# Kernel optimization log

Hardware: AMD Instinct MI355X
Metric: run time of the kernel (lower is better)

Reference implementation:

```python
import jax, jax.numpy as jnp
import numpy as np

N = 100000
E = 1600000
D_IN = 128
D_OUT = 128
EPS = 1e-5


def setup_inputs() -> dict:
    key = jax.random.key(0)
    ks = jax.random.split(key, 8)
    x = jax.random.normal(ks[0], (N, D_IN), dtype=jnp.float32)
    edge_index = jax.random.randint(ks[1], (2, E), 0, N, dtype=jnp.int64)
    s1 = 1.0 / np.sqrt(D_IN)
    s2 = 1.0 / np.sqrt(D_OUT)
    W1 = jax.random.uniform(ks[2], (D_IN, D_OUT), jnp.float32, -s1, s1)
    b1 = jax.random.uniform(ks[3], (D_OUT,), jnp.float32, -s1, s1)
    W2 = jax.random.uniform(ks[4], (D_OUT, D_OUT), jnp.float32, -s2, s2)
    b2 = jax.random.uniform(ks[5], (D_OUT,), jnp.float32, -s2, s2)
    gamma = jnp.ones((D_OUT,), jnp.float32)
    beta = jnp.zeros((D_OUT,), jnp.float32)
    return {"x": x, "edge_index": edge_index, "W1": W1, "b1": b1,
            "W2": W2, "b2": b2, "gamma": gamma, "beta": beta}


def reference(x, edge_index, W1, b1, W2, b2, gamma, beta):
    row, col = edge_index[0], edge_index[1]
    # scatter-add neighbor aggregation: agg[row] += x[col]
    agg = jax.ops.segment_sum(x[col], row, num_segments=N)
    h = x + agg  # residual (self) + aggregated neighbors
    # MLP: Linear -> ReLU -> Linear -> BatchNorm1d (training-mode batch stats)
    h = jax.nn.relu(h @ W1 + b1)
    h = h @ W2 + b2
    mean = jnp.mean(h, axis=0)
    var = jnp.mean(jnp.square(h - mean), axis=0)  # biased var, as torch BN uses
    out = gamma * (h - mean) * jax.lax.rsqrt(var + EPS) + beta
    return out
```

## Files before the change

### kernel.cpp

```cpp
#include <hip/hip_runtime.h>

#define N_NODES 100000
#define N_EDGES 1600000
#define DIM     128
#define EPS_BN  1e-5f
#define NB      512
#define NPB     196
#define NBLK    256
#define EPB     6250
#define CAP     4096
#define M_TILE  64
#define M_PAD   100032
#define GBLK    1563
#define LPITCH  136

typedef __attribute__((ext_vector_type(8))) short short8;
typedef __attribute__((ext_vector_type(4))) float floatx4;

__device__ __forceinline__ unsigned short f2bf(float f) {
    unsigned u = __float_as_uint(f);
    return (unsigned short)((u + 0x7FFF + ((u >> 16) & 1)) >> 16);
}
__device__ __forceinline__ float bf2f(unsigned short b) {
    return __uint_as_float((unsigned)b << 16);
}

__device__ __forceinline__ int detect64(const void* eidx) {
    int v = ((const int*)eidx)[2 * (threadIdx.x & 63) + 1];
    unsigned long long b = __ballot(v != 0);
    return (b == 0ULL) ? 1 : 0;
}
__device__ __forceinline__ int load_row(const void* eidx, int is64, int e) {
    if (is64) return (int)((const long long*)eidx)[e];
    return ((const int*)eidx)[e];
}
__device__ __forceinline__ int load_col(const void* eidx, int is64, int e) {
    if (is64) return (int)((const long long*)eidx)[N_EDGES + e];
    return ((const int*)eidx)[N_EDGES + e];
}

__global__ void convert_w(const float* __restrict__ W1,
                          const float* __restrict__ W2,
                          unsigned short* __restrict__ W1t,
                          unsigned short* __restrict__ W2t,
                          int* __restrict__ bcur, float* __restrict__ gstats) {
    if (blockIdx.x == 2) {
        int t = threadIdx.x;
        if (t < NB) bcur[t] = 0;
        if (t < 256) { if (t < NB - 256) bcur[256 + t] = 0; }
        bcur[256 + threadIdx.x] = 0;
        if (t < 2 * DIM) gstats[t] = 0.f;
        return;
    }
    const float* W = blockIdx.x ? W2 : W1;
    unsigned short* Wt = blockIdx.x ? W2t : W1t;
    for (int i = threadIdx.x; i < DIM * DIM; i += 256) {
        int k = i >> 7, n = i & 127;
        Wt[n * DIM + k] = f2bf(W[i]);
    }
}

__global__ __launch_bounds__(256) void bin_scatter(const void* eidx, int* bcur,
                                                   unsigned* __restrict__ slots) {
    __shared__ int lh[NB];
    __shared__ int lbase[NB];
    __shared__ int loff[NB];
    __shared__ unsigned stage[EPB];
    __shared__ int gaddr[EPB];
    int t = threadIdx.x;
    int is64 = detect64(eidx);
    lh[t] = 0; lh[t + 256] = 0;
    __syncthreads();
    int base = blockIdx.x * EPB;
    for (int i = t; i < EPB; i += 256) {
        int r = load_row(eidx, is64, base + i);
        atomicAdd(&lh[r / NPB], 1);
    }
    __syncthreads();
    loff[t] = lh[t]; loff[t + 256] = lh[t + 256];
    __syncthreads();
    for (int off = 1; off < NB; off <<= 1) {
        int a0 = (t >= off) ? loff[t - off] : 0;
        int a1 = (t + 256 >= off) ? loff[t + 256 - off] : 0;
        __syncthreads();
        loff[t] += a0; loff[t + 256] += a1;
        __syncthreads();
    }
#pragma unroll
    for (int q = 0; q < 2; ++q) {
        int i = t + 256 * q;
        int c = lh[i];
        lbase[i] = c ? atomicAdd(&bcur[i], c) : 0;
        loff[i] -= c;
        lh[i] = 0;
    }
    __syncthreads();
    for (int i = t; i < EPB; i += 256) {
        int r = load_row(eidx, is64, base + i);
        int c = load_col(eidx, is64, base + i);
        int b = r / NPB;
        int pos = atomicAdd(&lh[b], 1);
        int idx = loff[b] + pos;
        stage[idx] = ((unsigned)(r - b * NPB) << 24) | (unsigned)c;
        gaddr[idx] = b * CAP + lbase[b] + pos;
    }
    __syncthreads();
    for (int i = t; i < EPB; i += 256)
        slots[gaddr[i]] = stage[i];
}

__global__ __launch_bounds__(256) void build_csr(const unsigned* __restrict__ slots,
                                                 const int* __restrict__ bcnt,
                                                 int* __restrict__ rowst,
                                                 int* __restrict__ cols) {
    __shared__ int tmp[NB];
    __shared__ int hist[256];
    __shared__ int excl[256];
    __shared__ int cur[256];
    __shared__ int colbuf[CAP];
    int t = threadIdx.x;
    int b = blockIdx.x;
    tmp[t] = bcnt[t]; tmp[t + 256] = bcnt[t + 256];
    __syncthreads();
    for (int off = 1; off < NB; off <<= 1) {
        int a0 = (t >= off) ? tmp[t - off] : 0;
        int a1 = (t + 256 >= off) ? tmp[t + 256 - off] : 0;
        __syncthreads();
        tmp[t] += a0; tmp[t + 256] += a1;
        __syncthreads();
    }
    int cnt = bcnt[b];
    int s = tmp[b] - cnt;
    int node0 = b * NPB;
    int nn = N_NODES - node0;
    if (nn > NPB) nn = NPB;
    const unsigned* pairs = slots + (size_t)b * CAP;
    hist[t] = 0;
    if (b == NB - 1 && t == 0) rowst[N_NODES] = N_EDGES;
    __syncthreads();
    for (int i = t; i < cnt; i += 256)
        atomicAdd(&hist[(int)(pairs[i] >> 24)], 1);
    __syncthreads();
    int v = hist[t];
    excl[t] = v;
    __syncthreads();
    for (int off = 1; off < 256; off <<= 1) {
        int a = (t >= off) ? excl[t - off] : 0;
        __syncthreads();
        excl[t] += a;
        __syncthreads();
    }
    int ex = excl[t] - v;
    if (t < nn) rowst[node0 + t] = s + ex;
    cur[t] = ex;
    __syncthreads();
    for (int i = t; i < cnt; i += 256) {
        unsigned pr = pairs[i];
        int pos = atomicAdd(&cur[pr >> 24], 1);
        colbuf[pos] = (int)(pr & 0xFFFFFFu);
    }
    __syncthreads();
    for (int i = t; i < cnt; i += 256) cols[s + i] = colbuf[i];
}

__global__ void xconv(const float* __restrict__ x,
                      unsigned short* __restrict__ xb) {
    int i = blockIdx.x * 256 + threadIdx.x;
    float4 v = ((const float4*)x)[i];
    ushort4 o;
    o.x = f2bf(v.x); o.y = f2bf(v.y); o.z = f2bf(v.z); o.w = f2bf(v.w);
    ((ushort4*)xb)[i] = o;
}

__global__ __launch_bounds__(256) void agg_kernel(
    const unsigned short* __restrict__ xb,
    const int* __restrict__ row_start, const int* __restrict__ cols,
    unsigned short* __restrict__ Hbf) {
    int wave = threadIdx.x >> 6;
    int lane = threadIdx.x & 63;
    int node = blockIdx.x * 4 + wave;
    const unsigned* xbw = (const unsigned*)xb;
    unsigned selfw = xbw[(size_t)node * 64 + lane];
    float2 acc;
    acc.x = __uint_as_float(selfw << 16);
    acc.y = __uint_as_float(selfw & 0xffff0000u);
    int s = row_start[node], e = row_start[node + 1];
    s = __builtin_amdgcn_readfirstlane(s);
    e = __builtin_amdgcn_readfirstlane(e);
    int d = e - s;
    if (d <= 16) {
        unsigned pw[16];
#pragma unroll
        for (int u = 0; u < 16; ++u) {
            int idx = s + u;
            int ci = (idx < e) ? idx : s;
            pw[u] = xbw[(size_t)cols[ci] * 64 + lane];
        }
#pragma unroll
        for (int u = 0; u < 16; ++u) {
            unsigned w = (u < d) ? pw[u] : 0u;
            acc.x += __uint_as_float(w << 16);
            acc.y += __uint_as_float(w & 0xffff0000u);
        }
    } else if (d <= 32) {
        unsigned pw[32];
#pragma unroll
        for (int u = 0; u < 32; ++u) {
            int idx = s + u;
            int ci = (idx < e) ? idx : s;
            pw[u] = xbw[(size_t)cols[ci] * 64 + lane];
        }
#pragma unroll
        for (int u = 0; u < 32; ++u) {
            unsigned w = (u < d) ? pw[u] : 0u;
            acc.x += __uint_as_float(w << 16);
            acc.y += __uint_as_float(w & 0xffff0000u);
        }
    } else {
        int j = s;
        for (; j + 16 <= e; j += 16) {
            unsigned pw[16];
#pragma unroll
            for (int u = 0; u < 16; ++u)
                pw[u] = xbw[(size_t)cols[j + u] * 64 + lane];
#pragma unroll
            for (int u = 0; u < 16; ++u) {
                acc.x += __uint_as_float(pw[u] << 16);
                acc.y += __uint_as_float(pw[u] & 0xffff0000u);
            }
        }
        for (; j < e; ++j) {
            unsigned pv = xbw[(size_t)cols[j] * 64 + lane];
            acc.x += __uint_as_float(pv << 16);
            acc.y += __uint_as_float(pv & 0xffff0000u);
        }
    }
    unsigned pack = (unsigned)f2bf(acc.x) | ((unsigned)f2bf(acc.y) << 16);
    ((unsigned*)Hbf)[(size_t)node * 64 + lane] = pack;
}

__global__ __launch_bounds__(256) void mlp_fused(
    const unsigned short* __restrict__ A,
    const unsigned short* __restrict__ B1t,
    const unsigned short* __restrict__ B2t,
    const float* __restrict__ bias1, const float* __restrict__ bias2,
    unsigned short* __restrict__ outb,
    float* __restrict__ gpart) {
    __shared__ unsigned short As[M_TILE * LPITCH];
    __shared__ unsigned short Bs[DIM * LPITCH];
    int t = threadIdx.x;
    int row0 = blockIdx.x * M_TILE;
    int lane = t & 63, wv = t >> 6;
    int m = lane & 15, g = lane >> 4;

#pragma unroll
    for (int i = 0; i < 4; ++i) {
        int ch = t + 256 * i;
        int r = ch >> 4, cc = ch & 15;
        *(uint4*)(&As[r * LPITCH + cc * 8]) =
            *(const uint4*)(&A[(size_t)(row0 + r) * DIM + cc * 8]);
    }
#pragma unroll
    for (int i = 0; i < 8; ++i) {
        int ch = t + 256 * i;
        int n = ch >> 4, cc = ch & 15;
        *(uint4*)(&Bs[n * LPITCH + cc * 8]) =
            *(const uint4*)(&B1t[n * DIM + cc * 8]);
    }
    __syncthreads();

    floatx4 acc1[8] = {};
#pragma unroll
    for (int kc = 0; kc < 4; ++kc) {
        short8 a = *(const short8*)(&As[(wv * 16 + m) * LPITCH + kc * 32 + g * 8]);
#pragma unroll
        for (int tt = 0; tt < 8; ++tt) {
            short8 b = *(const short8*)(&Bs[(tt * 16 + m) * LPITCH + kc * 32 + g * 8]);
            acc1[tt] = __builtin_amdgcn_mfma_f32_16x16x32_bf16(a, b, acc1[tt], 0, 0, 0);
        }
    }
    __syncthreads();

    uint4 wbuf[8];
#pragma unroll
    for (int i = 0; i < 8; ++i) {
        int ch = t + 256 * i;
        int n = ch >> 4, cc = ch & 15;
        wbuf[i] = *(const uint4*)(&B2t[n * DIM + cc * 8]);
    }
#pragma unroll
    for (int tt = 0; tt < 8; ++tt) {
        int col = tt * 16 + m;
        float bv = bias1[col];
#pragma unroll
        for (int j = 0; j < 4; ++j) {
            int rl = wv * 16 + g * 4 + j;
            As[rl * LPITCH + col] = f2bf(fmaxf(acc1[tt][j] + bv, 0.f));
        }
    }
#pragma unroll
    for (int i = 0; i < 8; ++i) {
        int ch = t + 256 * i;
        int n = ch >> 4, cc = ch & 15;
        *(uint4*)(&Bs[n * LPITCH + cc * 8]) = wbuf[i];
    }
    __syncthreads();

    floatx4 acc2[8] = {};
#pragma unroll
    for (int kc = 0; kc < 4; ++kc) {
        short8 a = *(const short8*)(&As[(wv * 16 + m) * LPITCH + kc * 32 + g * 8]);
#pragma unroll
        for (int tt = 0; tt < 8; ++tt) {
            short8 b = *(const short8*)(&Bs[(tt * 16 + m) * LPITCH + kc * 32 + g * 8]);
            acc2[tt] = __builtin_amdgcn_mfma_f32_16x16x32_bf16(a, b, acc2[tt], 0, 0, 0);
        }
    }

    float* csum = (float*)As;
    float* csq = csum + DIM;
    __syncthreads();
    if (t < DIM) { csum[t] = 0.f; csq[t] = 0.f; }
    __syncthreads();
#pragma unroll
    for (int tt = 0; tt < 8; ++tt) {
        int col = tt * 16 + m;
        float bv = bias2[col];
        float s = 0.f, q = 0.f;
#pragma unroll
        for (int j = 0; j < 4; ++j) {
            int row = row0 + wv * 16 + g * 4 + j;
            float v = acc2[tt][j] + bv;
            outb[(size_t)row * DIM + col] = f2bf(v);
            if (row < N_NODES) { s += v; q += v * v; }
        }
        atomicAdd(&csum[col], s);
        atomicAdd(&csq[col], q);
    }
    __syncthreads();
    gpart[(size_t)blockIdx.x * 256 + t] = (t < DIM) ? csum[t] : csq[t - DIM];
}

__global__ __launch_bounds__(256) void reduce_stats(
    const float* __restrict__ gpart, float* __restrict__ gstats) {
    int t = threadIdx.x;
    int chunk = (GBLK + 31) / 32;
    int r0 = blockIdx.x * chunk;
    int r1 = r0 + chunk < GBLK ? r0 + chunk : GBLK;
    float s = 0.f;
    for (int r = r0; r < r1; ++r) s += gpart[(size_t)r * 256 + t];
    atomicAdd(&gstats[t], s);
}

__global__ __launch_bounds__(256) void bn_apply(
    const unsigned short* __restrict__ H2, const float* __restrict__ gstats,
    const float* __restrict__ gamma, const float* __restrict__ beta,
    float* __restrict__ out) {
    __shared__ float sc_s[DIM], sh_s[DIM];
    int t = threadIdx.x;
    if (t < DIM) {
        float mean = gstats[t] * (1.0f / N_NODES);
        float m2 = gstats[DIM + t] * (1.0f / N_NODES);
        float var = m2 - mean * mean;
        float inv = rsqrtf(var + EPS_BN);
        float sc = gamma[t] * inv;
        sc_s[t] = sc;
        sh_s[t] = beta[t] - mean * sc;
    }
    __syncthreads();
    int i = blockIdx.x * 256 + t;
    int j4 = (i & 31) * 4;
    ushort4 hv = ((const ushort4*)H2)[i];
    float4 o;
    o.x = bf2f(hv.x) * sc_s[j4 + 0] + sh_s[j4 + 0];
    o.y = bf2f(hv.y) * sc_s[j4 + 1] + sh_s[j4 + 1];
    o.z = bf2f(hv.z) * sc_s[j4 + 2] + sh_s[j4 + 2];
    o.w = bf2f(hv.w) * sc_s[j4 + 3] + sh_s[j4 + 3];
    ((float4*)out)[i] = o;
}

extern "C" void kernel_launch(void* const* d_in, const int* in_sizes, int n_in,
                              void* d_out, int out_size, void* d_ws,
                              size_t ws_size, hipStream_t stream) {
    (void)in_sizes; (void)n_in; (void)out_size; (void)ws_size;
    const float* x     = (const float*)d_in[0];
    const void*  eidx  = d_in[1];
    const float* W1    = (const float*)d_in[2];
    const float* b1    = (const float*)d_in[3];
    const float* W2    = (const float*)d_in[4];
    const float* b2    = (const float*)d_in[5];
    const float* gamma = (const float*)d_in[6];
    const float* beta  = (const float*)d_in[7];
    float* out = (float*)d_out;

    char* p = (char*)d_ws;
    auto alloc = [&](size_t bytes) {
        char* r = p;
        p += (bytes + 255) & ~(size_t)255;
        return r;
    };
    unsigned short* Hbf  = (unsigned short*)alloc((size_t)M_PAD * DIM * 2);
    unsigned short* h2bf = (unsigned short*)alloc((size_t)M_PAD * DIM * 2);
    unsigned* slots = (unsigned*)h2bf;
    unsigned short* xb = (unsigned short*)alloc((size_t)N_NODES * DIM * 2);
    int*   cols   = (int*)alloc((size_t)(N_EDGES + 64) * 4);
    float* gpart  = (float*)alloc((size_t)GBLK * 256 * 4);
    int*   rowst  = (int*)alloc((size_t)(N_NODES + 1) * 4);
    int*   bcur   = (int*)alloc(NB * 4);
    unsigned short* W1t = (unsigned short*)alloc(DIM * DIM * 2);
    unsigned short* W2t = (unsigned short*)alloc(DIM * DIM * 2);
    float* gstats = (float*)alloc(2 * DIM * 4);

    convert_w<<<3, 256, 0, stream>>>(W1, W2, W1t, W2t, bcur, gstats);
    bin_scatter<<<NBLK, 256, 0, stream>>>(eidx, bcur, slots);
    build_csr<<<NB, 256, 0, stream>>>(slots, bcur, rowst, cols);

    xconv<<<N_NODES * DIM / 4 / 256, 256, 0, stream>>>(x, xb);
    agg_kernel<<<N_NODES / 4, 256, 0, stream>>>(xb, rowst, cols, Hbf);

    mlp_fused<<<GBLK, 256, 0, stream>>>(Hbf, W1t, W2t, b1, b2, h2bf, gpart);
    reduce_stats<<<32, 256, 0, stream>>>(gpart, gstats);
    bn_apply<<<(N_NODES * DIM / 4) / 256, 256, 0, stream>>>(h2bf, gstats,
                                                            gamma, beta, out);
}
```

Baseline: 312.0 us.

## Fuse neighbor aggregation into MLP kernel and merge x and weight conversion

The CSR gather-aggregation now runs inside the MLP kernel: each wave aggregates 16 nodes one after another and writes the bf16 result straight into the LDS A-tile. This removes the intermediate Hbf buffer and its global write and read-back, plus one kernel launch. The x-to-bf16 conversion is also merged with the weight transpose and counter zeroing into one launch. In exchange, far fewer waves are in flight for the latency-bound gather (1563 blocks with a large LDS footprint instead of 25000 small blocks), and each wave's node loop is serial, which can hide memory latency less well.

```diff
diff --git a/kernel.cpp b/kernel.cpp
--- a/kernel.cpp
+++ b/kernel.cpp
@@ -39,24 +39,30 @@
     return ((const int*)eidx)[N_EDGES + e];
 }
 
-__global__ void convert_w(const float* __restrict__ W1,
-                          const float* __restrict__ W2,
-                          unsigned short* __restrict__ W1t,
-                          unsigned short* __restrict__ W2t,
-                          int* __restrict__ bcur, float* __restrict__ gstats) {
-    if (blockIdx.x == 2) {
+__global__ void xconv_w(const float* __restrict__ x,
+                        unsigned short* __restrict__ xb,
+                        const float* __restrict__ W1,
+                        const float* __restrict__ W2,
+                        unsigned short* __restrict__ W1t,
+                        unsigned short* __restrict__ W2t,
+                        int* __restrict__ bcur, float* __restrict__ gstats) {
+    int i = blockIdx.x * 256 + threadIdx.x;
+    float4 v = ((const float4*)x)[i];
+    ushort4 o;
+    o.x = f2bf(v.x); o.y = f2bf(v.y); o.z = f2bf(v.z); o.w = f2bf(v.w);
+    ((ushort4*)xb)[i] = o;
+    if (blockIdx.x < 2) {
+        const float* W = blockIdx.x ? W2 : W1;
+        unsigned short* Wt = blockIdx.x ? W2t : W1t;
+        for (int j = threadIdx.x; j < DIM * DIM; j += 256) {
+            int k = j >> 7, n = j & 127;
+            Wt[n * DIM + k] = f2bf(W[j]);
+        }
+    } else if (blockIdx.x == 2) {
         int t = threadIdx.x;
-        if (t < NB) bcur[t] = 0;
-        if (t < 256) { if (t < NB - 256) bcur[256 + t] = 0; }
-        bcur[256 + threadIdx.x] = 0;
+        bcur[t] = 0;
+        bcur[256 + t] = 0;
         if (t < 2 * DIM) gstats[t] = 0.f;
-        return;
-    }
-    const float* W = blockIdx.x ? W2 : W1;
-    unsigned short* Wt = blockIdx.x ? W2t : W1t;
-    for (int i = threadIdx.x; i < DIM * DIM; i += 256) {
-        int k = i >> 7, n = i & 127;
-        Wt[n * DIM + k] = f2bf(W[i]);
     }
 }
 
@@ -163,84 +169,9 @@
     for (int i = t; i < cnt; i += 256) cols[s + i] = colbuf[i];
 }
 
-__global__ void xconv(const float* __restrict__ x,
-                      unsigned short* __restrict__ xb) {
-    int i = blockIdx.x * 256 + threadIdx.x;
-    float4 v = ((const float4*)x)[i];
-    ushort4 o;
-    o.x = f2bf(v.x); o.y = f2bf(v.y); o.z = f2bf(v.z); o.w = f2bf(v.w);
-    ((ushort4*)xb)[i] = o;
-}
-
-__global__ __launch_bounds__(256) void agg_kernel(
+__global__ __launch_bounds__(256) void agg_mlp(
     const unsigned short* __restrict__ xb,
     const int* __restrict__ row_start, const int* __restrict__ cols,
-    unsigned short* __restrict__ Hbf) {
-    int wave = threadIdx.x >> 6;
-    int lane = threadIdx.x & 63;
-    int node = blockIdx.x * 4 + wave;
-    const unsigned* xbw = (const unsigned*)xb;
-    unsigned selfw = xbw[(size_t)node * 64 + lane];
-    float2 acc;
-    acc.x = __uint_as_float(selfw << 16);
-    acc.y = __uint_as_float(selfw & 0xffff0000u);
-    int s = row_start[node], e = row_start[node + 1];
-    s = __builtin_amdgcn_readfirstlane(s);
-    e = __builtin_amdgcn_readfirstlane(e);
-    int d = e - s;
-    if (d <= 16) {
-        unsigned pw[16];
-#pragma unroll
-        for (int u = 0; u < 16; ++u) {
-            int idx = s + u;
-            int ci = (idx < e) ? idx : s;
-            pw[u] = xbw[(size_t)cols[ci] * 64 + lane];
-        }
-#pragma unroll
-        for (int u = 0; u < 16; ++u) {
-            unsigned w = (u < d) ? pw[u] : 0u;
-            acc.x += __uint_as_float(w << 16);
-            acc.y += __uint_as_float(w & 0xffff0000u);
-        }
-    } else if (d <= 32) {
-        unsigned pw[32];
-#pragma unroll
-        for (int u = 0; u < 32; ++u) {
-            int idx = s + u;
-            int ci = (idx < e) ? idx : s;
-            pw[u] = xbw[(size_t)cols[ci] * 64 + lane];
-        }
-#pragma unroll
-        for (int u = 0; u < 32; ++u) {
-            unsigned w = (u < d) ? pw[u] : 0u;
-            acc.x += __uint_as_float(w << 16);
-            acc.y += __uint_as_float(w & 0xffff0000u);
-        }
-    } else {
-        int j = s;
-        for (; j + 16 <= e; j += 16) {
-            unsigned pw[16];
-#pragma unroll
-            for (int u = 0; u < 16; ++u)
-                pw[u] = xbw[(size_t)cols[j + u] * 64 + lane];
-#pragma unroll
-            for (int u = 0; u < 16; ++u) {
-                acc.x += __uint_as_float(pw[u] << 16);
-                acc.y += __uint_as_float(pw[u] & 0xffff0000u);
-            }
-        }
-        for (; j < e; ++j) {
-            unsigned pv = xbw[(size_t)cols[j] * 64 + lane];
-            acc.x += __uint_as_float(pv << 16);
-            acc.y += __uint_as_float(pv & 0xffff0000u);
-        }
-    }
-    unsigned pack = (unsigned)f2bf(acc.x) | ((unsigned)f2bf(acc.y) << 16);
-    ((unsigned*)Hbf)[(size_t)node * 64 + lane] = pack;
-}
-
-__global__ __launch_bounds__(256) void mlp_fused(
-    const unsigned short* __restrict__ A,
     const unsigned short* __restrict__ B1t,
     const unsigned short* __restrict__ B2t,
     const float* __restrict__ bias1, const float* __restrict__ bias2,
@@ -254,18 +185,76 @@
     int m = lane & 15, g = lane >> 4;
 
 #pragma unroll
-    for (int i = 0; i < 4; ++i) {
-        int ch = t + 256 * i;
-        int r = ch >> 4, cc = ch & 15;
-        *(uint4*)(&As[r * LPITCH + cc * 8]) =
-            *(const uint4*)(&A[(size_t)(row0 + r) * DIM + cc * 8]);
-    }
-#pragma unroll
     for (int i = 0; i < 8; ++i) {
         int ch = t + 256 * i;
         int n = ch >> 4, cc = ch & 15;
         *(uint4*)(&Bs[n * LPITCH + cc * 8]) =
             *(const uint4*)(&B1t[n * DIM + cc * 8]);
+    }
+
+    const unsigned* xbw = (const unsigned*)xb;
+    for (int r = 0; r < 16; ++r) {
+        int node = row0 + wv * 16 + r;
+        unsigned pack = 0u;
+        if (node < N_NODES) {
+            unsigned selfw = xbw[(size_t)node * 64 + lane];
+            float2 acc;
+            acc.x = __uint_as_float(selfw << 16);
+            acc.y = __uint_as_float(selfw & 0xffff0000u);
+            int s = row_start[node], e = row_start[node + 1];
+            s = __builtin_amdgcn_readfirstlane(s);
+            e = __builtin_amdgcn_readfirstlane(e);
+            int d = e - s;
+            if (d <= 16) {
+                unsigned pw[16];
+#pragma unroll
+                for (int u = 0; u < 16; ++u) {
+                    int idx = s + u;
+                    int ci = (idx < e) ? idx : s;
+                    pw[u] = xbw[(size_t)cols[ci] * 64 + lane];
+                }
+#pragma unroll
+                for (int u = 0; u < 16; ++u) {
+                    unsigned w = (u < d) ? pw[u] : 0u;
+                    acc.x += __uint_as_float(w << 16);
+                    acc.y += __uint_as_float(w & 0xffff0000u);
+                }
+            } else if (d <= 32) {
+                unsigned pw[32];
+#pragma unroll
+                for (int u = 0; u < 32; ++u) {
+                    int idx = s + u;
+                    int ci = (idx < e) ? idx : s;
+                    pw[u] = xbw[(size_t)cols[ci] * 64 + lane];
+                }
+#pragma unroll
+                for (int u = 0; u < 32; ++u) {
+                    unsigned w = (u < d) ? pw[u] : 0u;
+                    acc.x += __uint_as_float(w << 16);
+                    acc.y += __uint_as_float(w & 0xffff0000u);
+                }
+            } else {
+                int j = s;
+                for (; j + 16 <= e; j += 16) {
+                    unsigned pw[16];
+#pragma unroll
+                    for (int u = 0; u < 16; ++u)
+                        pw[u] = xbw[(size_t)cols[j + u] * 64 + lane];
+#pragma unroll
+                    for (int u = 0; u < 16; ++u) {
+                        acc.x += __uint_as_float(pw[u] << 16);
+                        acc.y += __uint_as_float(pw[u] & 0xffff0000u);
+                    }
+                }
+                for (; j < e; ++j) {
+                    unsigned pv = xbw[(size_t)cols[j] * 64 + lane];
+                    acc.x += __uint_as_float(pv << 16);
+                    acc.y += __uint_as_float(pv & 0xffff0000u);
+                }
+            }
+            pack = (unsigned)f2bf(acc.x) | ((unsigned)f2bf(acc.y) << 16);
+        }
+        *(unsigned*)(&As[(wv * 16 + r) * LPITCH + lane * 2]) = pack;
     }
     __syncthreads();
 
@@ -399,7 +388,6 @@
         p += (bytes + 255) & ~(size_t)255;
         return r;
     };
-    unsigned short* Hbf  = (unsigned short*)alloc((size_t)M_PAD * DIM * 2);
     unsigned short* h2bf = (unsigned short*)alloc((size_t)M_PAD * DIM * 2);
     unsigned* slots = (unsigned*)h2bf;
     unsigned short* xb = (unsigned short*)alloc((size_t)N_NODES * DIM * 2);
@@ -411,14 +399,13 @@
     unsigned short* W2t = (unsigned short*)alloc(DIM * DIM * 2);
     float* gstats = (float*)alloc(2 * DIM * 4);
 
-    convert_w<<<3, 256, 0, stream>>>(W1, W2, W1t, W2t, bcur, gstats);
+    xconv_w<<<N_NODES * DIM / 4 / 256, 256, 0, stream>>>(x, xb, W1, W2,
+                                                         W1t, W2t, bcur, gstats);
     bin_scatter<<<NBLK, 256, 0, stream>>>(eidx, bcur, slots);
     build_csr<<<NB, 256, 0, stream>>>(slots, bcur, rowst, cols);
 
-    xconv<<<N_NODES * DIM / 4 / 256, 256, 0, stream>>>(x, xb);
-    agg_kernel<<<N_NODES / 4, 256, 0, stream>>>(xb, rowst, cols, Hbf);
-
-    mlp_fused<<<GBLK, 256, 0, stream>>>(Hbf, W1t, W2t, b1, b2, h2bf, gpart);
+    agg_mlp<<<GBLK, 256, 0, stream>>>(xb, rowst, cols, W1t, W2t, b1, b2,
+                                      h2bf, gpart);
     reduce_stats<<<32, 256, 0, stream>>>(gpart, gstats);
     bn_apply<<<(N_NODES * DIM / 4) / 256, 256, 0, stream>>>(h2bf, gstats,
                                                             gamma, beta, out);
```

Result: slower. 326.4 us (+4.6%).

## Make MLP kernel persistent with prefetched tiles and fuse x conversion into binning

Applied to the files above, without the earlier changes.

The MLP kernel becomes persistent with 256 blocks. Each block loads both weight matrices into LDS once, double-buffers the A tiles with a register prefetch of the next tile, and accumulates BN statistics in registers across its tiles, so the reduce-stats pass has fewer partials. The separate x-to-bf16 conversion kernel is folded into the tail of the bin-scatter kernel to save one launch and overlap with the scatter work. In exchange, LDS use rises to about 104KB per block, which limits occupancy, and only 256 blocks may underfill the GPU's compute units.

```diff
diff --git a/kernel.cpp b/kernel.cpp
--- a/kernel.cpp
+++ b/kernel.cpp
@@ -12,6 +12,7 @@
 #define M_TILE  64
 #define M_PAD   100032
 #define GBLK    1563
+#define PBLK    256
 #define LPITCH  136
 
 typedef __attribute__((ext_vector_type(8))) short short8;
@@ -46,9 +47,8 @@
                           int* __restrict__ bcur, float* __restrict__ gstats) {
     if (blockIdx.x == 2) {
         int t = threadIdx.x;
-        if (t < NB) bcur[t] = 0;
-        if (t < 256) { if (t < NB - 256) bcur[256 + t] = 0; }
-        bcur[256 + threadIdx.x] = 0;
+        bcur[t] = 0;
+        bcur[256 + t] = 0;
         if (t < 2 * DIM) gstats[t] = 0.f;
         return;
     }
@@ -60,8 +60,9 @@
     }
 }
 
-__global__ __launch_bounds__(256) void bin_scatter(const void* eidx, int* bcur,
-                                                   unsigned* __restrict__ slots) {
+__global__ __launch_bounds__(256) void bin_scatter_x(
+    const void* eidx, int* bcur, unsigned* __restrict__ slots,
+    const float* __restrict__ x, unsigned short* __restrict__ xb) {
     __shared__ int lh[NB];
     __shared__ int lbase[NB];
     __shared__ int loff[NB];
@@ -107,6 +108,12 @@
     __syncthreads();
     for (int i = t; i < EPB; i += 256)
         slots[gaddr[i]] = stage[i];
+    for (int i = blockIdx.x * 256 + t; i < N_NODES * DIM / 4; i += NBLK * 256) {
+        float4 v = ((const float4*)x)[i];
+        ushort4 o;
+        o.x = f2bf(v.x); o.y = f2bf(v.y); o.z = f2bf(v.z); o.w = f2bf(v.w);
+        ((ushort4*)xb)[i] = o;
+    }
 }
 
 __global__ __launch_bounds__(256) void build_csr(const unsigned* __restrict__ slots,
@@ -161,15 +168,6 @@
     }
     __syncthreads();
     for (int i = t; i < cnt; i += 256) cols[s + i] = colbuf[i];
-}
-
-__global__ void xconv(const float* __restrict__ x,
-                      unsigned short* __restrict__ xb) {
-    int i = blockIdx.x * 256 + threadIdx.x;
-    float4 v = ((const float4*)x)[i];
-    ushort4 o;
-    o.x = f2bf(v.x); o.y = f2bf(v.y); o.z = f2bf(v.z); o.w = f2bf(v.w);
-    ((ushort4*)xb)[i] = o;
 }
 
 __global__ __launch_bounds__(256) void agg_kernel(
@@ -239,82 +237,105 @@
     ((unsigned*)Hbf)[(size_t)node * 64 + lane] = pack;
 }
 
-__global__ __launch_bounds__(256) void mlp_fused(
+__global__ __launch_bounds__(256) void mlp_persist(
     const unsigned short* __restrict__ A,
     const unsigned short* __restrict__ B1t,
     const unsigned short* __restrict__ B2t,
     const float* __restrict__ bias1, const float* __restrict__ bias2,
     unsigned short* __restrict__ outb,
     float* __restrict__ gpart) {
-    __shared__ unsigned short As[M_TILE * LPITCH];
-    __shared__ unsigned short Bs[DIM * LPITCH];
+    __shared__ unsigned short As[2][M_TILE * LPITCH];
+    __shared__ unsigned short Bs1[DIM * LPITCH];
+    __shared__ unsigned short Bs2[DIM * LPITCH];
     int t = threadIdx.x;
-    int row0 = blockIdx.x * M_TILE;
     int lane = t & 63, wv = t >> 6;
     int m = lane & 15, g = lane >> 4;
-
-#pragma unroll
-    for (int i = 0; i < 4; ++i) {
-        int ch = t + 256 * i;
-        int r = ch >> 4, cc = ch & 15;
-        *(uint4*)(&As[r * LPITCH + cc * 8]) =
-            *(const uint4*)(&A[(size_t)(row0 + r) * DIM + cc * 8]);
-    }
+    int r_ = t >> 4, c_ = t & 15;
+
 #pragma unroll
     for (int i = 0; i < 8; ++i) {
         int ch = t + 256 * i;
         int n = ch >> 4, cc = ch & 15;
-        *(uint4*)(&Bs[n * LPITCH + cc * 8]) =
-            *(const uint4*)(&B1t[n * DIM + cc * 8]);
-    }
-    __syncthreads();
-
-    floatx4 acc1[8] = {};
-#pragma unroll
-    for (int kc = 0; kc < 4; ++kc) {
-        short8 a = *(const short8*)(&As[(wv * 16 + m) * LPITCH + kc * 32 + g * 8]);
+        *(uint4*)(&Bs1[n * LPITCH + cc * 8]) = *(const uint4*)(&B1t[n * DIM + cc * 8]);
+        *(uint4*)(&Bs2[n * LPITCH + cc * 8]) = *(const uint4*)(&B2t[n * DIM + cc * 8]);
+    }
+    int tl = blockIdx.x;
+    {
+        int row0 = tl * M_TILE;
+#pragma unroll
+        for (int i = 0; i < 4; ++i)
+            *(uint4*)(&As[0][(r_ + 16 * i) * LPITCH + c_ * 8]) =
+                *(const uint4*)(&A[(size_t)(row0 + r_ + 16 * i) * DIM + c_ * 8]);
+    }
+    float bv1[8], bv2[8];
+#pragma unroll
+    for (int tt = 0; tt < 8; ++tt) {
+        bv1[tt] = bias1[tt * 16 + m];
+        bv2[tt] = bias2[tt * 16 + m];
+    }
+    float bsum[8] = {}, bsq[8] = {};
+    __syncthreads();
+
+    int cur = 0;
+    while (tl < GBLK) {
+        int nxt = tl + PBLK;
+        bool pf = (nxt < GBLK);
+        uint4 ald[4];
+        if (pf) {
+            int row0n = nxt * M_TILE;
+#pragma unroll
+            for (int i = 0; i < 4; ++i)
+                ald[i] = *(const uint4*)(&A[(size_t)(row0n + r_ + 16 * i) * DIM + c_ * 8]);
+        }
+        floatx4 acc1[8] = {};
+#pragma unroll
+        for (int kc = 0; kc < 4; ++kc) {
+            short8 a = *(const short8*)(&As[cur][(wv * 16 + m) * LPITCH + kc * 32 + g * 8]);
+#pragma unroll
+            for (int tt = 0; tt < 8; ++tt) {
+                short8 b = *(const short8*)(&Bs1[(tt * 16 + m) * LPITCH + kc * 32 + g * 8]);
+                acc1[tt] = __builtin_amdgcn_mfma_f32_16x16x32_bf16(a, b, acc1[tt], 0, 0, 0);
+            }
+        }
+        __syncthreads();
 #pragma unroll
         for (int tt = 0; tt < 8; ++tt) {
-            short8 b = *(const short8*)(&Bs[(tt * 16 + m) * LPITCH + kc * 32 + g * 8]);
-            acc1[tt] = __builtin_amdgcn_mfma_f32_16x16x32_bf16(a, b, acc1[tt], 0, 0, 0);
-        }
-    }
-    __syncthreads();
-
-    uint4 wbuf[8];
-#pragma unroll
-    for (int i = 0; i < 8; ++i) {
-        int ch = t + 256 * i;
-        int n = ch >> 4, cc = ch & 15;
-        wbuf[i] = *(const uint4*)(&B2t[n * DIM + cc * 8]);
-    }
-#pragma unroll
-    for (int tt = 0; tt < 8; ++tt) {
-        int col = tt * 16 + m;
-        float bv = bias1[col];
-#pragma unroll
-        for (int j = 0; j < 4; ++j) {
-            int rl = wv * 16 + g * 4 + j;
-            As[rl * LPITCH + col] = f2bf(fmaxf(acc1[tt][j] + bv, 0.f));
-        }
-    }
-#pragma unroll
-    for (int i = 0; i < 8; ++i) {
-        int ch = t + 256 * i;
-        int n = ch >> 4, cc = ch & 15;
-        *(uint4*)(&Bs[n * LPITCH + cc * 8]) = wbuf[i];
-    }
-    __syncthreads();
-
-    floatx4 acc2[8] = {};
-#pragma unroll
-    for (int kc = 0; kc < 4; ++kc) {
-        short8 a = *(const short8*)(&As[(wv * 16 + m) * LPITCH + kc * 32 + g * 8]);
+            int col = tt * 16 + m;
+#pragma unroll
+            for (int j = 0; j < 4; ++j) {
+                int rl = wv * 16 + g * 4 + j;
+                As[cur][rl * LPITCH + col] = f2bf(fmaxf(acc1[tt][j] + bv1[tt], 0.f));
+            }
+        }
+        if (pf) {
+#pragma unroll
+            for (int i = 0; i < 4; ++i)
+                *(uint4*)(&As[cur ^ 1][(r_ + 16 * i) * LPITCH + c_ * 8]) = ald[i];
+        }
+        __syncthreads();
+        floatx4 acc2[8] = {};
+#pragma unroll
+        for (int kc = 0; kc < 4; ++kc) {
+            short8 a = *(const short8*)(&As[cur][(wv * 16 + m) * LPITCH + kc * 32 + g * 8]);
+#pragma unroll
+            for (int tt = 0; tt < 8; ++tt) {
+                short8 b = *(const short8*)(&Bs2[(tt * 16 + m) * LPITCH + kc * 32 + g * 8]);
+                acc2[tt] = __builtin_amdgcn_mfma_f32_16x16x32_bf16(a, b, acc2[tt], 0, 0, 0);
+            }
+        }
+        int row0 = tl * M_TILE;
 #pragma unroll
         for (int tt = 0; tt < 8; ++tt) {
-            short8 b = *(const short8*)(&Bs[(tt * 16 + m) * LPITCH + kc * 32 + g * 8]);
-            acc2[tt] = __builtin_amdgcn_mfma_f32_16x16x32_bf16(a, b, acc2[tt], 0, 0, 0);
-        }
+            int col = tt * 16 + m;
+#pragma unroll
+            for (int j = 0; j < 4; ++j) {
+                int row = row0 + wv * 16 + g * 4 + j;
+                float v = acc2[tt][j] + bv2[tt];
+                outb[(size_t)row * DIM + col] = f2bf(v);
+                if (row < N_NODES) { bsum[tt] += v; bsq[tt] += v * v; }
+            }
+        }
+        tl = nxt; cur ^= 1;
     }
 
     float* csum = (float*)As;
@@ -324,18 +345,8 @@
     __syncthreads();
 #pragma unroll
     for (int tt = 0; tt < 8; ++tt) {
-        int col = tt * 16 + m;
-        float bv = bias2[col];
-        float s = 0.f, q = 0.f;
-#pragma unroll
-        for (int j = 0; j < 4; ++j) {
-            int row = row0 + wv * 16 + g * 4 + j;
-            float v = acc2[tt][j] + bv;
-            outb[(size_t)row * DIM + col] = f2bf(v);
-            if (row < N_NODES) { s += v; q += v * v; }
-        }
-        atomicAdd(&csum[col], s);
-        atomicAdd(&csq[col], q);
+        atomicAdd(&csum[tt * 16 + m], bsum[tt]);
+        atomicAdd(&csq[tt * 16 + m], bsq[tt]);
     }
     __syncthreads();
     gpart[(size_t)blockIdx.x * 256 + t] = (t < DIM) ? csum[t] : csq[t - DIM];
@@ -344,11 +355,9 @@
 __global__ __launch_bounds__(256) void reduce_stats(
     const float* __restrict__ gpart, float* __restrict__ gstats) {
     int t = threadIdx.x;
-    int chunk = (GBLK + 31) / 32;
-    int r0 = blockIdx.x * chunk;
-    int r1 = r0 + chunk < GBLK ? r0 + chunk : GBLK;
+    int r0 = blockIdx.x * (PBLK / 32);
     float s = 0.f;
-    for (int r = r0; r < r1; ++r) s += gpart[(size_t)r * 256 + t];
+    for (int r = r0; r < r0 + PBLK / 32; ++r) s += gpart[(size_t)r * 256 + t];
     atomicAdd(&gstats[t], s);
 }
 
@@ -404,7 +413,7 @@
     unsigned* slots = (unsigned*)h2bf;
     unsigned short* xb = (unsigned short*)alloc((size_t)N_NODES * DIM * 2);
     int*   cols   = (int*)alloc((size_t)(N_EDGES + 64) * 4);
-    float* gpart  = (float*)alloc((size_t)GBLK * 256 * 4);
+    float* gpart  = (float*)alloc((size_t)PBLK * 256 * 4);
     int*   rowst  = (int*)alloc((size_t)(N_NODES + 1) * 4);
     int*   bcur   = (int*)alloc(NB * 4);
     unsigned short* W1t = (unsigned short*)alloc(DIM * DIM * 2);
@@ -412,13 +421,12 @@
     float* gstats = (float*)alloc(2 * DIM * 4);
 
     convert_w<<<3, 256, 0, stream>>>(W1, W2, W1t, W2t, bcur, gstats);
-    bin_scatter<<<NBLK, 256, 0, stream>>>(eidx, bcur, slots);
+    bin_scatter_x<<<NBLK, 256, 0, stream>>>(eidx, bcur, slots, x, xb);
     build_csr<<<NB, 256, 0, stream>>>(slots, bcur, rowst, cols);
 
-    xconv<<<N_NODES * DIM / 4 / 256, 256, 0, stream>>>(x, xb);
     agg_kernel<<<N_NODES / 4, 256, 0, stream>>>(xb, rowst, cols, Hbf);
 
-    mlp_fused<<<GBLK, 256, 0, stream>>>(Hbf, W1t, W2t, b1, b2, h2bf, gpart);
+    mlp_persist<<<PBLK, 256, 0, stream>>>(Hbf, W1t, W2t, b1, b2, h2bf, gpart);
     reduce_stats<<<32, 256, 0, stream>>>(gpart, gstats);
     bn_apply<<<(N_NODES * DIM / 4) / 256, 256, 0, stream>>>(h2bf, gstats,
                                                             gamma, beta, out);
```

Result: no change. 309.2 us (-0.9%).

## Replace bucketed CSR build with degree histogram, scan, and atomic scatter

Applied to the files above, without the earlier changes.

Replaces the two-pass bucket binning CSR construction (shared-memory staging into fixed-capacity slots, then a per-bucket local sort) with a global per-node degree histogram via atomics, a two-kernel prefix scan, and a direct atomic scatter of column indices. The x-to-bf16 conversion, weight transposition and zeroing are folded into a single init kernel. The aim is to cut the staged buffer traffic and shared-memory-heavy low-occupancy kernels. In exchange it relies on 1.6M global atomics on random addresses, and the order of neighbours within a row becomes nondeterministic.

```diff
diff --git a/kernel.cpp b/kernel.cpp
--- a/kernel.cpp
+++ b/kernel.cpp
@@ -4,15 +4,12 @@
 #define N_EDGES 1600000
 #define DIM     128
 #define EPS_BN  1e-5f
-#define NB      512
-#define NPB     196
-#define NBLK    256
-#define EPB     6250
-#define CAP     4096
 #define M_TILE  64
 #define M_PAD   100032
 #define GBLK    1563
 #define LPITCH  136
+#define EGRID   2048
+#define CHUNK   391
 
 typedef __attribute__((ext_vector_type(8))) short short8;
 typedef __attribute__((ext_vector_type(4))) float floatx4;
@@ -39,137 +36,113 @@
     return ((const int*)eidx)[N_EDGES + e];
 }
 
-__global__ void convert_w(const float* __restrict__ W1,
-                          const float* __restrict__ W2,
-                          unsigned short* __restrict__ W1t,
-                          unsigned short* __restrict__ W2t,
-                          int* __restrict__ bcur, float* __restrict__ gstats) {
-    if (blockIdx.x == 2) {
-        int t = threadIdx.x;
-        if (t < NB) bcur[t] = 0;
-        if (t < 256) { if (t < NB - 256) bcur[256 + t] = 0; }
-        bcur[256 + threadIdx.x] = 0;
+__global__ __launch_bounds__(256) void init_all(
+    const float* __restrict__ x, unsigned short* __restrict__ xb,
+    const float* __restrict__ W1, const float* __restrict__ W2,
+    unsigned short* __restrict__ W1t, unsigned short* __restrict__ W2t,
+    int* __restrict__ deg, float* __restrict__ gstats) {
+    int t = threadIdx.x;
+    for (int i = blockIdx.x * 256 + t; i < N_NODES * DIM / 4; i += EGRID * 256) {
+        float4 v = ((const float4*)x)[i];
+        ushort4 o;
+        o.x = f2bf(v.x); o.y = f2bf(v.y); o.z = f2bf(v.z); o.w = f2bf(v.w);
+        ((ushort4*)xb)[i] = o;
+    }
+    if (blockIdx.x < 2) {
+        const float* W = blockIdx.x ? W2 : W1;
+        unsigned short* Wt = blockIdx.x ? W2t : W1t;
+        for (int j = t; j < DIM * DIM; j += 256) {
+            int k = j >> 7, n = j & 127;
+            Wt[n * DIM + k] = f2bf(W[j]);
+        }
+    } else if (blockIdx.x == 2) {
         if (t < 2 * DIM) gstats[t] = 0.f;
-        return;
-    }
-    const float* W = blockIdx.x ? W2 : W1;
-    unsigned short* Wt = blockIdx.x ? W2t : W1t;
-    for (int i = threadIdx.x; i < DIM * DIM; i += 256) {
-        int k = i >> 7, n = i & 127;
-        Wt[n * DIM + k] = f2bf(W[i]);
-    }
-}
-
-__global__ __launch_bounds__(256) void bin_scatter(const void* eidx, int* bcur,
-                                                   unsigned* __restrict__ slots) {
-    __shared__ int lh[NB];
-    __shared__ int lbase[NB];
-    __shared__ int loff[NB];
-    __shared__ unsigned stage[EPB];
-    __shared__ int gaddr[EPB];
-    int t = threadIdx.x;
+    } else if (blockIdx.x >= 3 && blockIdx.x < 103) {
+        int base = (blockIdx.x - 3) * 1024;
+#pragma unroll
+        for (int k = 0; k < 4; ++k) {
+            int i = base + k * 256 + t;
+            if (i < N_NODES) deg[i] = 0;
+        }
+    }
+}
+
+__global__ __launch_bounds__(256) void edge_hist(const void* eidx,
+                                                 int* __restrict__ deg) {
     int is64 = detect64(eidx);
-    lh[t] = 0; lh[t + 256] = 0;
-    __syncthreads();
-    int base = blockIdx.x * EPB;
-    for (int i = t; i < EPB; i += 256) {
-        int r = load_row(eidx, is64, base + i);
-        atomicAdd(&lh[r / NPB], 1);
-    }
-    __syncthreads();
-    loff[t] = lh[t]; loff[t + 256] = lh[t + 256];
-    __syncthreads();
-    for (int off = 1; off < NB; off <<= 1) {
-        int a0 = (t >= off) ? loff[t - off] : 0;
-        int a1 = (t + 256 >= off) ? loff[t + 256 - off] : 0;
+    for (int e = blockIdx.x * 256 + threadIdx.x; e < N_EDGES; e += EGRID * 256)
+        atomicAdd(&deg[load_row(eidx, is64, e)], 1);
+}
+
+__global__ __launch_bounds__(256) void scan_part(const int* __restrict__ deg,
+                                                 int* __restrict__ bsum) {
+    __shared__ int red[256];
+    int t = threadIdx.x;
+    int n0 = blockIdx.x * CHUNK;
+    int s = 0;
+    int i0 = n0 + t, i1 = n0 + t + 256;
+    if (t < CHUNK && i0 < N_NODES) s += deg[i0];
+    if (t + 256 < CHUNK && i1 < N_NODES) s += deg[i1];
+    red[t] = s;
+    __syncthreads();
+    for (int off = 128; off > 0; off >>= 1) {
+        if (t < off) red[t] += red[t + off];
         __syncthreads();
-        loff[t] += a0; loff[t + 256] += a1;
+    }
+    if (t == 0) bsum[blockIdx.x] = red[0];
+}
+
+__global__ __launch_bounds__(256) void scan_write(const int* __restrict__ deg,
+                                                  const int* __restrict__ bsum,
+                                                  int* __restrict__ rowst,
+                                                  int* __restrict__ cur) {
+    __shared__ int bs[256];
+    __shared__ int ch[512];
+    int t = threadIdx.x;
+    int b = blockIdx.x;
+    bs[t] = bsum[t];
+    __syncthreads();
+    for (int off = 1; off < 256; off <<= 1) {
+        int a = (t >= off) ? bs[t - off] : 0;
         __syncthreads();
-    }
-#pragma unroll
-    for (int q = 0; q < 2; ++q) {
-        int i = t + 256 * q;
-        int c = lh[i];
-        lbase[i] = c ? atomicAdd(&bcur[i], c) : 0;
-        loff[i] -= c;
-        lh[i] = 0;
-    }
-    __syncthreads();
-    for (int i = t; i < EPB; i += 256) {
-        int r = load_row(eidx, is64, base + i);
-        int c = load_col(eidx, is64, base + i);
-        int b = r / NPB;
-        int pos = atomicAdd(&lh[b], 1);
-        int idx = loff[b] + pos;
-        stage[idx] = ((unsigned)(r - b * NPB) << 24) | (unsigned)c;
-        gaddr[idx] = b * CAP + lbase[b] + pos;
-    }
-    __syncthreads();
-    for (int i = t; i < EPB; i += 256)
-        slots[gaddr[i]] = stage[i];
-}
-
-__global__ __launch_bounds__(256) void build_csr(const unsigned* __restrict__ slots,
-                                                 const int* __restrict__ bcnt,
-                                                 int* __restrict__ rowst,
-                                                 int* __restrict__ cols) {
-    __shared__ int tmp[NB];
-    __shared__ int hist[256];
-    __shared__ int excl[256];
-    __shared__ int cur[256];
-    __shared__ int colbuf[CAP];
-    int t = threadIdx.x;
-    int b = blockIdx.x;
-    tmp[t] = bcnt[t]; tmp[t + 256] = bcnt[t + 256];
-    __syncthreads();
-    for (int off = 1; off < NB; off <<= 1) {
-        int a0 = (t >= off) ? tmp[t - off] : 0;
-        int a1 = (t + 256 >= off) ? tmp[t + 256 - off] : 0;
+        bs[t] += a;
         __syncthreads();
-        tmp[t] += a0; tmp[t + 256] += a1;
+    }
+    int base = (b == 0) ? 0 : bs[b - 1];
+    int n0 = b * CHUNK;
+    int v0 = 0, v1 = 0;
+    if (t < CHUNK && n0 + t < N_NODES) v0 = deg[n0 + t];
+    if (t + 256 < CHUNK && n0 + t + 256 < N_NODES) v1 = deg[n0 + t + 256];
+    ch[t] = v0; ch[t + 256] = v1;
+    __syncthreads();
+    for (int off = 1; off < 512; off <<= 1) {
+        int a0 = (t >= off) ? ch[t - off] : 0;
+        int a1 = (t + 256 >= off) ? ch[t + 256 - off] : 0;
         __syncthreads();
-    }
-    int cnt = bcnt[b];
-    int s = tmp[b] - cnt;
-    int node0 = b * NPB;
-    int nn = N_NODES - node0;
-    if (nn > NPB) nn = NPB;
-    const unsigned* pairs = slots + (size_t)b * CAP;
-    hist[t] = 0;
-    if (b == NB - 1 && t == 0) rowst[N_NODES] = N_EDGES;
-    __syncthreads();
-    for (int i = t; i < cnt; i += 256)
-        atomicAdd(&hist[(int)(pairs[i] >> 24)], 1);
-    __syncthreads();
-    int v = hist[t];
-    excl[t] = v;
-    __syncthreads();
-    for (int off = 1; off < 256; off <<= 1) {
-        int a = (t >= off) ? excl[t - off] : 0;
+        ch[t] += a0; ch[t + 256] += a1;
         __syncthreads();
-        excl[t] += a;
-        __syncthreads();
-    }
-    int ex = excl[t] - v;
-    if (t < nn) rowst[node0 + t] = s + ex;
-    cur[t] = ex;
-    __syncthreads();
-    for (int i = t; i < cnt; i += 256) {
-        unsigned pr = pairs[i];
-        int pos = atomicAdd(&cur[pr >> 24], 1);
-        colbuf[pos] = (int)(pr & 0xFFFFFFu);
-    }
-    __syncthreads();
-    for (int i = t; i < cnt; i += 256) cols[s + i] = colbuf[i];
-}
-
-__global__ void xconv(const float* __restrict__ x,
-                      unsigned short* __restrict__ xb) {
-    int i = blockIdx.x * 256 + threadIdx.x;
-    float4 v = ((const float4*)x)[i];
-    ushort4 o;
-    o.x = f2bf(v.x); o.y = f2bf(v.y); o.z = f2bf(v.z); o.w = f2bf(v.w);
-    ((ushort4*)xb)[i] = o;
+    }
+    if (t < CHUNK && n0 + t < N_NODES) {
+        int e = base + ch[t] - v0;
+        rowst[n0 + t] = e; cur[n0 + t] = e;
+    }
+    if (t + 256 < CHUNK && n0 + t + 256 < N_NODES) {
+        int e = base + ch[t + 256] - v1;
+        rowst[n0 + t + 256] = e; cur[n0 + t + 256] = e;
+    }
+    if (b == 255 && t == 0) rowst[N_NODES] = N_EDGES;
+}
+
+__global__ __launch_bounds__(256) void scatter_cols(const void* eidx,
+                                                    int* __restrict__ cur,
+                                                    int* __restrict__ cols) {
+    int is64 = detect64(eidx);
+    for (int e = blockIdx.x * 256 + threadIdx.x; e < N_EDGES; e += EGRID * 256) {
+        int r = load_row(eidx, is64, e);
+        int c = load_col(eidx, is64, e);
+        int pos = atomicAdd(&cur[r], 1);
+        cols[pos] = c;
+    }
 }
 
 __global__ __launch_bounds__(256) void agg_kernel(
@@ -401,21 +374,23 @@
     };
     unsigned short* Hbf  = (unsigned short*)alloc((size_t)M_PAD * DIM * 2);
     unsigned short* h2bf = (unsigned short*)alloc((size_t)M_PAD * DIM * 2);
-    unsigned* slots = (unsigned*)h2bf;
     unsigned short* xb = (unsigned short*)alloc((size_t)N_NODES * DIM * 2);
     int*   cols   = (int*)alloc((size_t)(N_EDGES + 64) * 4);
     float* gpart  = (float*)alloc((size_t)GBLK * 256 * 4);
     int*   rowst  = (int*)alloc((size_t)(N_NODES + 1) * 4);
-    int*   bcur   = (int*)alloc(NB * 4);
     unsigned short* W1t = (unsigned short*)alloc(DIM * DIM * 2);
     unsigned short* W2t = (unsigned short*)alloc(DIM * DIM * 2);
     float* gstats = (float*)alloc(2 * DIM * 4);
-
-    convert_w<<<3, 256, 0, stream>>>(W1, W2, W1t, W2t, bcur, gstats);
-    bin_scatter<<<NBLK, 256, 0, stream>>>(eidx, bcur, slots);
-    build_csr<<<NB, 256, 0, stream>>>(slots, bcur, rowst, cols);
-
-    xconv<<<N_NODES * DIM / 4 / 256, 256, 0, stream>>>(x, xb);
+    int*   bsum   = (int*)alloc(256 * 4);
+    int* deg = (int*)gpart;
+    int* cur = deg + 100352;
+
+    init_all<<<EGRID, 256, 0, stream>>>(x, xb, W1, W2, W1t, W2t, deg, gstats);
+    edge_hist<<<EGRID, 256, 0, stream>>>(eidx, deg);
+    scan_part<<<256, 256, 0, stream>>>(deg, bsum);
+    scan_write<<<256, 256, 0, stream>>>(deg, bsum, rowst, cur);
+    scatter_cols<<<EGRID, 256, 0, stream>>>(eidx, cur, cols);
+
     agg_kernel<<<N_NODES / 4, 256, 0, stream>>>(xb, rowst, cols, Hbf);
 
     mlp_fused<<<GBLK, 256, 0, stream>>>(Hbf, W1t, W2t, b1, b2, h2bf, gpart);
```

After: 465.1 us. +49.1%, slower.
